# Kernel optimization log

Measured on AMD Instinct MI355X. Metric: run time of the kernel, lower is better.

The kernel has to match this reference:

```python
import jax, jax.numpy as jnp
import numpy as np

H = W = 512
A = 256  # number of projection angles


def setup_inputs() -> dict:
    key = jax.random.key(0)
    k1, k2 = jax.random.split(key)
    data = jax.random.normal(k1, (1, 1, H, W), dtype=jnp.float32)
    # angles uniform in [0, pi) -- realistic tomographic scan range
    angles = jax.random.uniform(k2, (A,), dtype=jnp.float32) * np.float32(np.pi)
    return {"data": data, "angles": angles}


def _radon(data, angles):
    B, C, h, w = data.shape  # B == C == 1 structurally required by the torch module
    nA = angles.shape[0]
    cos = jnp.cos(angles)
    sin = jnp.sin(angles)

    # F.affine_grid(align_corners=False) base coordinates: pixel centers in [-1, 1]
    xs = (2.0 * jnp.arange(w, dtype=data.dtype) + 1.0) / w - 1.0  # [W]
    ys = (2.0 * jnp.arange(h, dtype=data.dtype) + 1.0) / h - 1.0  # [H]
    by, bx = jnp.meshgrid(ys, xs, indexing="ij")  # [H,W]

    # theta built from -angles: rows [cos a, sin a, 0; -sin a, cos a, 0]
    gx = cos[:, None, None] * bx + sin[:, None, None] * by  # [A,H,W]
    gy = -sin[:, None, None] * bx + cos[:, None, None] * by  # [A,H,W]

    # grid_sample(align_corners=False): unnormalize to input pixel coords
    ix = ((gx + 1.0) * w - 1.0) * 0.5
    iy = ((gy + 1.0) * h - 1.0) * 0.5

    x0 = jnp.floor(ix).astype(jnp.int32)
    y0 = jnp.floor(iy).astype(jnp.int32)
    x1 = x0 + 1
    y1 = y0 + 1
    wx1 = ix - x0.astype(data.dtype)
    wx0 = 1.0 - wx1
    wy1 = iy - y0.astype(data.dtype)
    wy0 = 1.0 - wy1

    img = data[0, 0]  # [H,W]

    def gather(yy, xx):
        # zero padding: out-of-range taps contribute 0
        valid = (xx >= 0) & (xx < w) & (yy >= 0) & (yy < h)
        v = img[jnp.clip(yy, 0, h - 1), jnp.clip(xx, 0, w - 1)]
        return jnp.where(valid, v, jnp.zeros((), data.dtype))

    rotated = (wy0 * (wx0 * gather(y0, x0) + wx1 * gather(y0, x1))
               + wy1 * (wx0 * gather(y1, x0) + wx1 * gather(y1, x1)))  # [A,H,W]

    proj = jnp.sum(rotated, axis=1)  # sum over height -> [A,W]
    return proj.reshape(1, 1, nA, w)


def reference(data, angles):
    return _radon(data, angles)
```

## Files before the change

kernel.cpp:

```cpp
#include <hip/hip_runtime.h>


#define HH 512
#define WW 512
#define NA 256
#define XC 64
#define YC 64
#define NXC (WW / XC)
#define NYC (HH / YC)
#define NW 8
#define ROWS_MAX 92
#define SMAX 97
#define PAD 112
#define PW (WW + 2 * PAD)
#define PH (HH + 2 * PAD)

typedef float f32x2 __attribute__((ext_vector_type(2)));

__global__ __launch_bounds__(256) void pad_kernel(
    const float* __restrict__ img, float* __restrict__ P)
{
    const int c = blockIdx.x * 256 + threadIdx.x;
    const int r = blockIdx.y;
    if (c >= PW) return;
    const int gr = r - PAD, gc = c - PAD;
    float v = 0.0f;
    if ((unsigned)gr < (unsigned)HH && (unsigned)gc < (unsigned)WW)
        v = img[gr * WW + gc];
    P[r * PW + c] = v;
}

__device__ __forceinline__ float fract_f(float x) {
#if __has_builtin(__builtin_amdgcn_fractf)
    return __builtin_amdgcn_fractf(x);
#else
    return x - floorf(x);
#endif
}

template <int STRIDE>
__device__ __forceinline__ void sample_chunk(
    const float* __restrict__ tb, const int c_lo, const int r_lo, const float v0,
    const float s, const float c, const float u, const int wid,
    f32x2& accA, f32x2& accB)
{
    const float bc = fmaf(c, u, 255.5f - (float)c_lo);
    const float br = fmaf(-s, u, 255.5f - (float)r_lo);
    const float vy0 = v0 + (float)(wid * 8);

    f32x2 base, stepv;
    base.x = fmaf(s, vy0, bc);
    base.y = fmaf(c, vy0, br);
    stepv.x = s;
    stepv.y = c;

    f32x2 k2, k3, k4;
    k2.x = 2.0f; k2.y = 2.0f;
    k3.x = 3.0f; k3.y = 3.0f;
    k4.x = 4.0f; k4.y = 4.0f;

#pragma unroll
    for (int g = 0; g < 2; ++g) {
        f32x2 crs[4];
        crs[0] = base;
        crs[1] = base + stepv;
        crs[2] = __builtin_elementwise_fma(stepv, k2, base);
        crs[3] = __builtin_elementwise_fma(stepv, k3, base);
        base = __builtin_elementwise_fma(stepv, k4, base);

        int ad[4];
        float wx[4], wy[4];
#pragma unroll
        for (int i = 0; i < 4; ++i) {
            const int ci = (int)crs[i].x;
            const int ri = (int)crs[i].y;
            wx[i] = fract_f(crs[i].x);
            wy[i] = fract_f(crs[i].y);
            __builtin_assume(ri >= 0 && ri < ROWS_MAX);
            __builtin_assume(ci >= 0 && ci < SMAX);
            ad[i] = ri * STRIDE + ci;
        }

        f32x2 top[4], bot[4];
#pragma unroll
        for (int i = 0; i < 4; ++i) {
            top[i].x = tb[ad[i]];
            top[i].y = tb[ad[i] + 1];
            bot[i].x = tb[ad[i] + STRIDE];
            bot[i].y = tb[ad[i] + STRIDE + 1];
        }
        __builtin_amdgcn_sched_barrier(0);

        __builtin_amdgcn_s_setprio(1);
#pragma unroll
        for (int i = 0; i < 4; ++i) {
            f32x2 wyv;
            wyv.x = wy[i];
            wyv.y = wy[i];
            const f32x2 pv = __builtin_elementwise_fma(wyv, bot[i] - top[i], top[i]);
            f32x2 wxv;
            wxv.x = 1.0f - wx[i];
            wxv.y = wx[i];
            if (i & 1) accB = __builtin_elementwise_fma(wxv, pv, accB);
            else       accA = __builtin_elementwise_fma(wxv, pv, accA);
        }
        __builtin_amdgcn_s_setprio(0);
    }
}

template <bool PADDED, int STRIDE>
__device__ __forceinline__ void radon_body(
    const float* __restrict__ src, float* __restrict__ tile,
    const float s, const float c, const int lane, const int wid, const int x0,
    f32x2& accA, f32x2& accB)
{
    constexpr bool CPOS = (STRIDE == 95);

    const float u  = (float)(x0 + lane) + (0.5f - 256.0f);
    const float u0 = (float)x0 + (0.5f - 256.0f);
    const float u1 = u0 + (float)(XC - 1);

    const float* __restrict__ Porg = PADDED ? (src + PAD * PW + PAD) : src;

    for (int yc = 0; yc < NYC; ++yc) {
        const float v0 = (float)(yc * YC) + (0.5f - 256.0f);
        const float v1 = v0 + (float)(YC - 1);

        float cx_min, cx_max, rx_min, rx_max;
        if (CPOS) {
            cx_min = fmaf(c, u0, fmaf(s, v0, 255.5f));
            cx_max = fmaf(c, u1, fmaf(s, v1, 255.5f));
            rx_min = fmaf(-s, u1, fmaf(c, v0, 255.5f));
            rx_max = fmaf(-s, u0, fmaf(c, v1, 255.5f));
        } else {
            cx_min = fmaf(c, u1, fmaf(s, v0, 255.5f));
            cx_max = fmaf(c, u0, fmaf(s, v1, 255.5f));
            rx_min = fmaf(-s, u1, fmaf(c, v1, 255.5f));
            rx_max = fmaf(-s, u0, fmaf(c, v0, 255.5f));
        }

        const int c_lo = (int)floorf(cx_min);
        const int c_hi = (int)floorf(cx_max) + 1;
        const int r_lo = (int)floorf(rx_min);
        const int r_hi = (int)floorf(rx_max) + 1;
        const int bh = min(r_hi - r_lo + 1, ROWS_MAX);

        if (c_lo > WW - 1 || c_hi < 0 || r_lo > HH - 1 || r_hi < 0) continue;

        __syncthreads();

        if (PADDED) {
            if (lane < 23) {
                const float* g = Porg + (r_lo + wid) * PW + c_lo + lane * 4;
                float* l = &tile[wid * STRIDE];
                for (int r = wid; r < bh; r += NW) {
                    __builtin_amdgcn_global_load_lds(
                        (__attribute__((address_space(1))) const void*)g,
                        (__attribute__((address_space(3))) void*)l, 16, 0, 0);
                    g += NW * PW;
                    l += NW * STRIDE;
                }
            }
        } else {
            const int bw = min(c_hi - c_lo + 1, SMAX);
            for (int r = wid; r < bh; r += NW) {
                const int gr = r_lo + r;
                const bool row_ok = ((unsigned)gr < (unsigned)HH);
                const float* __restrict__ rowp = src + gr * WW;
                for (int cc = lane; cc < bw; cc += 64) {
                    const int gc = c_lo + cc;
                    float v = 0.0f;
                    if (row_ok) {
                        const int gcl = min(max(gc, 0), WW - 1);
                        const float t = rowp[gcl];
                        v = ((unsigned)gc < (unsigned)WW) ? t : 0.0f;
                    }
                    tile[r * STRIDE + cc] = v;
                }
            }
        }

        __syncthreads();

        sample_chunk<STRIDE>(tile, c_lo, r_lo, v0, s, c, u, wid, accA, accB);
    }
}

template <bool PADDED>
__global__ __launch_bounds__(512, 8) void radon_kernel(
    const float* __restrict__ src,
    const float* __restrict__ angles, float* __restrict__ out)
{
    __shared__ float tile[ROWS_MAX * SMAX];

    const int tid  = threadIdx.x;
    const int lane = tid & 63;
    const int wid  = tid >> 6;

    const int a  = blockIdx.x >> 3;
    const int x0 = (blockIdx.x & 7) * XC;

    float s, c;
    sincosf(angles[a], &s, &c);

    f32x2 accA, accB;
    accA.x = 0.0f; accA.y = 0.0f;
    accB.x = 0.0f; accB.y = 0.0f;
    if (c >= 0.0f)
        radon_body<PADDED, 95>(src, tile, s, c, lane, wid, x0, accA, accB);
    else
        radon_body<PADDED, 97>(src, tile, s, c, lane, wid, x0, accA, accB);

    __syncthreads();
    tile[tid] = (accA.x + accB.x) + (accA.y + accB.y);
    __syncthreads();
    if (tid < 64) {
        float r = tile[tid];
#pragma unroll
        for (int k = 1; k < NW; ++k) r += tile[k * 64 + tid];
        out[a * WW + x0 + tid] = r;
    }
}

extern "C" void kernel_launch(void* const* d_in, const int* in_sizes, int n_in,
                              void* d_out, int out_size, void* d_ws, size_t ws_size,
                              hipStream_t stream) {
    const float* img    = (const float*)d_in[0];
    const float* angles = (const float*)d_in[1];
    float* out = (float*)d_out;
    float* P   = (float*)d_ws;

    const bool padded = (ws_size >= (size_t)PW * PH * sizeof(float));

    if (padded) {
        pad_kernel<<<dim3((PW + 255) / 256, PH), 256, 0, stream>>>(img, P);
        radon_kernel<true><<<dim3(NA * NXC), 512, 0, stream>>>(P, angles, out);
    } else {
        radon_kernel<false><<<dim3(NA * NXC), 512, 0, stream>>>(img, angles, out);
    }
}
```

Before: 108.1 us.

## Sample bilinear taps directly from global memory instead of staging LDS tiles

Removes the per-chunk LDS tile staging (global_load_lds copies plus two block barriers per y-chunk) and has each thread gather its four bilinear taps straight from the padded global image. It relies on L1/L2 caching of the small image instead of explicit shared-memory reuse. This saves barrier and copy overhead but turns cheap LDS reads into scattered global loads with higher latency. The unpadded fallback path is also rewritten to gather directly with bounds checks.

After: 245.5 us. 127% more time.

```diff
diff --git a/kernel.cpp b/kernel.cpp
--- a/kernel.cpp
+++ b/kernel.cpp
@@ -5,12 +5,8 @@
 #define WW 512
 #define NA 256
 #define XC 64
-#define YC 64
 #define NXC (WW / XC)
-#define NYC (HH / YC)
 #define NW 8
-#define ROWS_MAX 92
-#define SMAX 97
 #define PAD 112
 #define PW (WW + 2 * PAD)
 #define PH (HH + 2 * PAD)
@@ -38,160 +34,12 @@
 #endif
 }
 
-template <int STRIDE>
-__device__ __forceinline__ void sample_chunk(
-    const float* __restrict__ tb, const int c_lo, const int r_lo, const float v0,
-    const float s, const float c, const float u, const int wid,
-    f32x2& accA, f32x2& accB)
-{
-    const float bc = fmaf(c, u, 255.5f - (float)c_lo);
-    const float br = fmaf(-s, u, 255.5f - (float)r_lo);
-    const float vy0 = v0 + (float)(wid * 8);
-
-    f32x2 base, stepv;
-    base.x = fmaf(s, vy0, bc);
-    base.y = fmaf(c, vy0, br);
-    stepv.x = s;
-    stepv.y = c;
-
-    f32x2 k2, k3, k4;
-    k2.x = 2.0f; k2.y = 2.0f;
-    k3.x = 3.0f; k3.y = 3.0f;
-    k4.x = 4.0f; k4.y = 4.0f;
-
-#pragma unroll
-    for (int g = 0; g < 2; ++g) {
-        f32x2 crs[4];
-        crs[0] = base;
-        crs[1] = base + stepv;
-        crs[2] = __builtin_elementwise_fma(stepv, k2, base);
-        crs[3] = __builtin_elementwise_fma(stepv, k3, base);
-        base = __builtin_elementwise_fma(stepv, k4, base);
-
-        int ad[4];
-        float wx[4], wy[4];
-#pragma unroll
-        for (int i = 0; i < 4; ++i) {
-            const int ci = (int)crs[i].x;
-            const int ri = (int)crs[i].y;
-            wx[i] = fract_f(crs[i].x);
-            wy[i] = fract_f(crs[i].y);
-            __builtin_assume(ri >= 0 && ri < ROWS_MAX);
-            __builtin_assume(ci >= 0 && ci < SMAX);
-            ad[i] = ri * STRIDE + ci;
-        }
-
-        f32x2 top[4], bot[4];
-#pragma unroll
-        for (int i = 0; i < 4; ++i) {
-            top[i].x = tb[ad[i]];
-            top[i].y = tb[ad[i] + 1];
-            bot[i].x = tb[ad[i] + STRIDE];
-            bot[i].y = tb[ad[i] + STRIDE + 1];
-        }
-        __builtin_amdgcn_sched_barrier(0);
-
-        __builtin_amdgcn_s_setprio(1);
-#pragma unroll
-        for (int i = 0; i < 4; ++i) {
-            f32x2 wyv;
-            wyv.x = wy[i];
-            wyv.y = wy[i];
-            const f32x2 pv = __builtin_elementwise_fma(wyv, bot[i] - top[i], top[i]);
-            f32x2 wxv;
-            wxv.x = 1.0f - wx[i];
-            wxv.y = wx[i];
-            if (i & 1) accB = __builtin_elementwise_fma(wxv, pv, accB);
-            else       accA = __builtin_elementwise_fma(wxv, pv, accA);
-        }
-        __builtin_amdgcn_s_setprio(0);
-    }
-}
-
-template <bool PADDED, int STRIDE>
-__device__ __forceinline__ void radon_body(
-    const float* __restrict__ src, float* __restrict__ tile,
-    const float s, const float c, const int lane, const int wid, const int x0,
-    f32x2& accA, f32x2& accB)
-{
-    constexpr bool CPOS = (STRIDE == 95);
-
-    const float u  = (float)(x0 + lane) + (0.5f - 256.0f);
-    const float u0 = (float)x0 + (0.5f - 256.0f);
-    const float u1 = u0 + (float)(XC - 1);
-
-    const float* __restrict__ Porg = PADDED ? (src + PAD * PW + PAD) : src;
-
-    for (int yc = 0; yc < NYC; ++yc) {
-        const float v0 = (float)(yc * YC) + (0.5f - 256.0f);
-        const float v1 = v0 + (float)(YC - 1);
-
-        float cx_min, cx_max, rx_min, rx_max;
-        if (CPOS) {
-            cx_min = fmaf(c, u0, fmaf(s, v0, 255.5f));
-            cx_max = fmaf(c, u1, fmaf(s, v1, 255.5f));
-            rx_min = fmaf(-s, u1, fmaf(c, v0, 255.5f));
-            rx_max = fmaf(-s, u0, fmaf(c, v1, 255.5f));
-        } else {
-            cx_min = fmaf(c, u1, fmaf(s, v0, 255.5f));
-            cx_max = fmaf(c, u0, fmaf(s, v1, 255.5f));
-            rx_min = fmaf(-s, u1, fmaf(c, v1, 255.5f));
-            rx_max = fmaf(-s, u0, fmaf(c, v0, 255.5f));
-        }
-
-        const int c_lo = (int)floorf(cx_min);
-        const int c_hi = (int)floorf(cx_max) + 1;
-        const int r_lo = (int)floorf(rx_min);
-        const int r_hi = (int)floorf(rx_max) + 1;
-        const int bh = min(r_hi - r_lo + 1, ROWS_MAX);
-
-        if (c_lo > WW - 1 || c_hi < 0 || r_lo > HH - 1 || r_hi < 0) continue;
-
-        __syncthreads();
-
-        if (PADDED) {
-            if (lane < 23) {
-                const float* g = Porg + (r_lo + wid) * PW + c_lo + lane * 4;
-                float* l = &tile[wid * STRIDE];
-                for (int r = wid; r < bh; r += NW) {
-                    __builtin_amdgcn_global_load_lds(
-                        (__attribute__((address_space(1))) const void*)g,
-                        (__attribute__((address_space(3))) void*)l, 16, 0, 0);
-                    g += NW * PW;
-                    l += NW * STRIDE;
-                }
-            }
-        } else {
-            const int bw = min(c_hi - c_lo + 1, SMAX);
-            for (int r = wid; r < bh; r += NW) {
-                const int gr = r_lo + r;
-                const bool row_ok = ((unsigned)gr < (unsigned)HH);
-                const float* __restrict__ rowp = src + gr * WW;
-                for (int cc = lane; cc < bw; cc += 64) {
-                    const int gc = c_lo + cc;
-                    float v = 0.0f;
-                    if (row_ok) {
-                        const int gcl = min(max(gc, 0), WW - 1);
-                        const float t = rowp[gcl];
-                        v = ((unsigned)gc < (unsigned)WW) ? t : 0.0f;
-                    }
-                    tile[r * STRIDE + cc] = v;
-                }
-            }
-        }
-
-        __syncthreads();
-
-        sample_chunk<STRIDE>(tile, c_lo, r_lo, v0, s, c, u, wid, accA, accB);
-    }
-}
-
 template <bool PADDED>
 __global__ __launch_bounds__(512, 8) void radon_kernel(
     const float* __restrict__ src,
     const float* __restrict__ angles, float* __restrict__ out)
 {
-    __shared__ float tile[ROWS_MAX * SMAX];
+    __shared__ float red[512];
 
     const int tid  = threadIdx.x;
     const int lane = tid & 63;
@@ -203,21 +51,119 @@
     float s, c;
     sincosf(angles[a], &s, &c);
 
+    const float u   = (float)(x0 + lane) + (0.5f - 256.0f);
+    const float cu  = c * u;
+    const float msu = -s * u;
+
     f32x2 accA, accB;
     accA.x = 0.0f; accA.y = 0.0f;
     accB.x = 0.0f; accB.y = 0.0f;
-    if (c >= 0.0f)
-        radon_body<PADDED, 95>(src, tile, s, c, lane, wid, x0, accA, accB);
-    else
-        radon_body<PADDED, 97>(src, tile, s, c, lane, wid, x0, accA, accB);
 
-    __syncthreads();
-    tile[tid] = (accA.x + accB.x) + (accA.y + accB.y);
+    if (PADDED) {
+        const float CK  = 255.5f + (float)PAD;
+        const float bcx = cu + CK;
+        const float bcy = msu + CK;
+
+        f32x2 stepv, k2, k3, k4;
+        stepv.x = s;   stepv.y = c;
+        k2.x = 2.0f; k2.y = 2.0f;
+        k3.x = 3.0f; k3.y = 3.0f;
+        k4.x = 4.0f; k4.y = 4.0f;
+
+#pragma unroll 1
+        for (int yc = 0; yc < 8; ++yc) {
+            const float vy0 = (float)(yc * 64 + wid * 8) - 255.5f;
+            f32x2 crx;
+            crx.x = fmaf(s, vy0, bcx);
+            crx.y = fmaf(c, vy0, bcy);
+
+#pragma unroll
+            for (int g = 0; g < 2; ++g) {
+                f32x2 crs[4];
+                crs[0] = crx;
+                crs[1] = crx + stepv;
+                crs[2] = __builtin_elementwise_fma(stepv, k2, crx);
+                crs[3] = __builtin_elementwise_fma(stepv, k3, crx);
+                crx = __builtin_elementwise_fma(stepv, k4, crx);
+
+                int ad[4];
+                float wx[4], wy[4];
+#pragma unroll
+                for (int i = 0; i < 4; ++i) {
+                    const int ci = (int)crs[i].x;
+                    const int ri = (int)crs[i].y;
+                    wx[i] = fract_f(crs[i].x);
+                    wy[i] = fract_f(crs[i].y);
+                    __builtin_assume(ci >= 0 && ci < PW - 1);
+                    __builtin_assume(ri >= 0 && ri < PH - 1);
+                    ad[i] = ri * PW + ci;
+                }
+
+                f32x2 top[4], bot[4];
+#pragma unroll
+                for (int i = 0; i < 4; ++i) {
+                    top[i].x = src[ad[i]];
+                    top[i].y = src[ad[i] + 1];
+                    bot[i].x = src[ad[i] + PW];
+                    bot[i].y = src[ad[i] + PW + 1];
+                }
+
+#pragma unroll
+                for (int i = 0; i < 4; ++i) {
+                    f32x2 wyv;
+                    wyv.x = wy[i];
+                    wyv.y = wy[i];
+                    const f32x2 pv =
+                        __builtin_elementwise_fma(wyv, bot[i] - top[i], top[i]);
+                    f32x2 wxv;
+                    wxv.x = 1.0f - wx[i];
+                    wxv.y = wx[i];
+                    if (i & 1) accB = __builtin_elementwise_fma(wxv, pv, accB);
+                    else       accA = __builtin_elementwise_fma(wxv, pv, accA);
+                }
+            }
+        }
+    } else {
+        const float bcx = cu + 255.5f;
+        const float bcy = msu + 255.5f;
+#pragma unroll 1
+        for (int yc = 0; yc < 8; ++yc) {
+            const float vy0 = (float)(yc * 64 + wid * 8) - 255.5f;
+#pragma unroll
+            for (int i = 0; i < 8; ++i) {
+                const float vy = vy0 + (float)i;
+                const float cx = fmaf(s, vy, bcx);
+                const float cy = fmaf(c, vy, bcy);
+                const float xf = floorf(cx);
+                const float yf = floorf(cy);
+                const float wx1 = cx - xf;
+                const float wy1 = cy - yf;
+                const int xi = (int)xf;
+                const int yi = (int)yf;
+                auto tap = [&](int yy, int xx) -> float {
+                    const bool ok = ((unsigned)xx < (unsigned)WW) &
+                                    ((unsigned)yy < (unsigned)HH);
+                    const int yyc = min(max(yy, 0), HH - 1);
+                    const int xxc = min(max(xx, 0), WW - 1);
+                    const float t = src[yyc * WW + xxc];
+                    return ok ? t : 0.0f;
+                };
+                const float v00 = tap(yi, xi),     v01 = tap(yi, xi + 1);
+                const float v10 = tap(yi + 1, xi), v11 = tap(yi + 1, xi + 1);
+                const float px0 = v00 + wy1 * (v10 - v00);
+                const float px1 = v01 + wy1 * (v11 - v01);
+                accA.x += (1.0f - wx1) * px0;
+                accA.y += wx1 * px1;
+            }
+        }
+    }
+
+    red[tid] = (accA.x + accB.x) + (accA.y + accB.y);
     __syncthreads();
     if (tid < 64) {
-        float r = tile[tid];
+        float r = red[tid];
 #pragma unroll
-        for (int k = 1; k < NW; ++k) r += tile[k * 64 + tid];
+        for (int k = 1; k < NW; ++k) r += red[k * 64 + tid];
         out[a * WW + x0 + tid] = r;
     }
 }
```
